# Optimization experiments

Hardware: AMD Instinct MI355X
Metric: run time of the kernel (lower is better)

The kernel has to match this reference:

```python
import jax, jax.numpy as jnp
import numpy as np

B, P, K = 32, 2048, 16
NHID, NCLS = 128, 10

def setup_inputs() -> dict:
    key = jax.random.key(0)
    ks = jax.random.split(key, 8)
    def w(k, shape):
        fan_in = shape[0]
        return jax.random.normal(k, shape, jnp.float32) / np.sqrt(fan_in)
    pos = jax.random.normal(ks[0], (B * P, 3), jnp.float32)
    batch = jnp.repeat(jnp.arange(B, dtype=jnp.int32), P)
    return dict(
        pos=pos, batch=batch,
        W1a=w(ks[1], (3 + 3, NHID)), b1a=jnp.zeros((NHID,), jnp.float32),
        W1b=w(ks[2], (NHID, NHID)), b1b=jnp.zeros((NHID,), jnp.float32),
        W2a=w(ks[3], (NHID + 3, NHID)), b2a=jnp.zeros((NHID,), jnp.float32),
        W2b=w(ks[4], (NHID, NHID)), b2b=jnp.zeros((NHID,), jnp.float32),
        Wc=w(ks[5], (NHID, NCLS)), bc=jnp.zeros((NCLS,), jnp.float32),
    )

def _gather(x, idx):
    # x: [B,P,C], idx: [B,P,K] -> [B,P,K,C]
    return jax.vmap(lambda xb, ib: xb[ib])(x, idx)

def _knn(posb):
    # posb: [B,P,3]; k nearest (incl. self, loop=True) per node -> [B,P,K]
    sq = jnp.sum(posb * posb, axis=-1)                      # [B,P]
    d2 = sq[:, :, None] + sq[:, None, :] - 2.0 * jnp.einsum('bpd,bqd->bpq', posb, posb)
    _, nbr = jax.lax.top_k(-d2, K)                          # [B,P,K]
    return nbr

def _pointnet_layer(h, posb, nbr, Wa, ba, Wb, bb):
    # message: concat(h_j, pos_j - pos_i) -> Linear -> ReLU -> Linear; aggr = max over K
    h_j = _gather(h, nbr)                                   # [B,P,K,C]
    rel = _gather(posb, nbr) - posb[:, :, None, :]          # [B,P,K,3]
    m = jnp.concatenate([h_j, rel], axis=-1)                # [B,P,K,C+3]
    m = jax.nn.relu(jnp.einsum('bpkc,cd->bpkd', m, Wa) + ba)
    m = jnp.einsum('bpkc,cd->bpkd', m, Wb) + bb
    return jnp.max(m, axis=2)                               # [B,P,NHID]

def reference(pos, batch, W1a, b1a, W1b, b1b, W2a, b2a, W2b, b2b, Wc, bc):
    posb = pos.reshape(B, P, 3)                             # batch is sorted, equal-size graphs
    nbr = _knn(posb)
    h = jax.nn.relu(_pointnet_layer(posb, posb, nbr, W1a, b1a, W1b, b1b))
    h = jax.nn.relu(_pointnet_layer(h, posb, nbr, W2a, b2a, W2b, b2b))
    g = jnp.max(h, axis=1)                                  # global_max_pool -> [B,NHID]
    return g @ Wc + bc                                      # [B,NCLS]
```

## Files before the change

### kernel.cpp

```cpp
#include <hip/hip_runtime.h>


typedef __bf16 bf16x8 __attribute__((ext_vector_type(8)));
typedef float  f32x4  __attribute__((ext_vector_type(4)));

#define LDSA __attribute__((aligned(16)))
#define WAVE_LDS_SYNC() __asm__ volatile("s_waitcnt lgkmcnt(0)" ::: "memory")

__global__ __launch_bounds__(512) void knn_kernel(const float* __restrict__ pos,
                                                  int* __restrict__ nbr) {
  __shared__ LDSA float4 P4[2048];
  const int blk = blockIdx.x;
  const int b = blk >> 5;
  const int tid = threadIdx.x;
  const size_t bbase = (size_t)b * 2048;
  for (int idx = tid; idx < 2048; idx += 512) {
    const float* pp = pos + (bbase + idx) * 3;
    float x = pp[0], y = pp[1], z = pp[2];
    P4[idx] = make_float4(-2.0f * x, -2.0f * y, -2.0f * z, fmaf(z, z, fmaf(y, y, x * x)));
  }
  __syncthreads();
  const int wave = tid >> 6, lane = tid & 63;
  const int p0 = (blk & 31) * 64 + wave * 8;
  const unsigned long long below = (1ull << lane) - 1ull;
  const float FINF = __uint_as_float(0x7F800000u);
  for (int it = 0; it < 8; ++it) {
    const int pl = p0 + it;
    const float4 Qp = P4[pl];
    const float Px = -0.5f * Qp.x, Py = -0.5f * Qp.y, Pz = -0.5f * Qp.z;
    float m1 = FINF, m2 = FINF, m3 = FINF;
    unsigned s1 = 0, s2 = 0, s3 = 0;
#pragma unroll 8
    for (int i = 0; i < 32; ++i) {
      int c = lane + (i << 6);
      float4 Q = P4[c];
      float d2 = fmaf(Px, Q.x, fmaf(Py, Q.y, fmaf(Pz, Q.z, Q.w)));
      bool c1 = d2 < m1, c2 = d2 < m2, c3 = d2 < m3;
      float n3 = __builtin_amdgcn_fmed3f(d2, m2, m3);
      float n2 = __builtin_amdgcn_fmed3f(d2, m1, m2);
      float n1 = fminf(d2, m1);
      s3 = c2 ? s2 : (c3 ? (unsigned)c : s3);
      s2 = c1 ? s1 : (c2 ? (unsigned)c : s2);
      s1 = c1 ? (unsigned)c : s1;
      m1 = n1; m2 = n2; m3 = n3;
    }
    unsigned u;
    unsigned k1, k2, k3;
    u = __float_as_uint(m1); k1 = ((int)u < 0) ? ~u : (u | 0x80000000u);
    u = __float_as_uint(m2); k2 = ((int)u < 0) ? ~u : (u | 0x80000000u);
    u = __float_as_uint(m3); k3 = ((int)u < 0) ? ~u : (u | 0x80000000u);
    unsigned v = 0;
#pragma unroll
    for (int bit = 31; bit >= 0; --bit) {
      unsigned t = v | (1u << bit);
      int cnt = __popcll(__ballot(k1 < t)) + __popcll(__ballot(k2 < t)) +
                __popcll(__ballot(k3 < t));
      if (cnt < 16) v = t;
    }
    const unsigned V = v;
    const long long outbase = ((long long)bbase + pl) * 16;
    if (__any(k3 < V)) {
      unsigned long long K1 = ((unsigned long long)k1 << 32) | s1;
      unsigned long long K2 = ((unsigned long long)k2 << 32) | s2;
      unsigned long long K3 = ((unsigned long long)k3 << 32) | s3;
      unsigned long long lastk = 0;
      for (int r = 0; r < 16; ++r) {
        unsigned long long k = K1, kmin = K1;
#pragma unroll
        for (int off = 1; off < 64; off <<= 1) {
          unsigned long long o = __shfl_xor(kmin, off);
          kmin = (o < kmin) ? o : kmin;
        }
        if (lane == r) nbr[outbase + r] = (int)(kmin & 0xFFFFFFFFull);
        if (k == kmin) { lastk = k; K1 = K2; K2 = K3; K3 = ~0ull; }
        if (r < 15 && __any(K1 == ~0ull)) {
          if (K1 == ~0ull) {
            unsigned long long best = ~0ull;
            for (int i = 0; i < 32; ++i) {
              int c = lane + (i << 6);
              float4 Q = P4[c];
              float d2 = fmaf(Px, Q.x, fmaf(Py, Q.y, fmaf(Pz, Q.z, Q.w)));
              unsigned uu = __float_as_uint(d2);
              uu = ((int)uu < 0) ? ~uu : (uu | 0x80000000u);
              unsigned long long kc = ((unsigned long long)uu << 32) | (unsigned)c;
              bool ok = (kc > lastk) & (kc < best);
              best = ok ? kc : best;
            }
            K1 = best;
          }
        }
      }
    } else {
      unsigned long long L1 = __ballot(k1 < V), L2 = __ballot(k2 < V), L3 = __ballot(k3 < V);
      unsigned long long E1 = __ballot(k1 == V), E2 = __ballot(k2 == V), E3 = __ballot(k3 == V);
      int cA = __popcll(L1), cB = cA + __popcll(L2), cT = cB + __popcll(L3);
      int eA = __popcll(E1), eB = eA + __popcll(E2);
      {
        bool lt = k1 < V, eq = k1 == V;
        int plt = __popcll(L1 & below);
        int peq = cT + __popcll(E1 & below);
        int p = lt ? plt : peq;
        if (lt || (eq && peq < 16)) nbr[outbase + p] = (int)s1;
      }
      {
        bool lt = k2 < V, eq = k2 == V;
        int plt = cA + __popcll(L2 & below);
        int peq = cT + eA + __popcll(E2 & below);
        int p = lt ? plt : peq;
        if (lt || (eq && peq < 16)) nbr[outbase + p] = (int)s2;
      }
      {
        bool lt = k3 < V, eq = k3 == V;
        int plt = cB + __popcll(L3 & below);
        int peq = cT + eB + __popcll(E3 & below);
        int p = lt ? plt : peq;
        if (lt || (eq && peq < 16)) nbr[outbase + p] = (int)s3;
      }
    }
  }
}

__global__ __launch_bounds__(256, 2) void layer1_kernel(
    const float* __restrict__ pos, const int* __restrict__ nbr,
    const float* __restrict__ W1a, const float* __restrict__ b1a,
    const float* __restrict__ W1b, const float* __restrict__ b1b,
    __bf16* __restrict__ h1e) {
  __shared__ LDSA char smem[34816];
  __bf16* Wbt = (__bf16*)smem;
  const int tid = threadIdx.x;
  for (int idx = tid; idx < 16384; idx += 256) {
    int k = idx >> 7, n = idx & 127;
    Wbt[n * 136 + k] = (__bf16)W1b[idx];
  }
  __syncthreads();
  const int wave = tid >> 6, lane = tid & 63;
  const int q = lane >> 4, c15 = lane & 15;
  bf16x8 bfr[8][4];
#pragma unroll
  for (int nt = 0; nt < 8; ++nt)
#pragma unroll
    for (int t = 0; t < 4; ++t)
      bfr[nt][t] = *(const bf16x8*)&Wbt[(nt * 16 + c15) * 136 + t * 32 + q * 8];
  __syncthreads();
  __bf16* mt = (__bf16*)smem + wave * 2176;
  float* base = (float*)(smem + 17408) + wave * 128;
  const int cb = lane & 7, k0 = lane >> 3, C0 = cb * 16;
  float4 s0h[4], s1h[4], s2h[4];
#pragma unroll
  for (int i = 0; i < 4; ++i) {
    float4 a0 = *(const float4*)&W1a[      C0 + 4 * i], r0 = *(const float4*)&W1a[384 + C0 + 4 * i];
    float4 a1 = *(const float4*)&W1a[128 + C0 + 4 * i], r1 = *(const float4*)&W1a[512 + C0 + 4 * i];
    float4 a2 = *(const float4*)&W1a[256 + C0 + 4 * i], r2 = *(const float4*)&W1a[640 + C0 + 4 * i];
    s0h[i] = make_float4(a0.x + r0.x, a0.y + r0.y, a0.z + r0.z, a0.w + r0.w);
    s1h[i] = make_float4(a1.x + r1.x, a1.y + r1.y, a1.z + r1.z, a1.w + r1.w);
    s2h[i] = make_float4(a2.x + r2.x, a2.y + r2.y, a2.z + r2.z, a2.w + r2.w);
  }
  const int c2 = lane * 2;
  const float br0a = W1a[384 + c2], br0b = W1a[384 + c2 + 1];
  const float br1a = W1a[512 + c2], br1b = W1a[512 + c2 + 1];
  const float br2a = W1a[640 + c2], br2b = W1a[640 + c2 + 1];
  const float ba0 = b1a[c2], ba1 = b1a[c2 + 1];
  const float bbi0 = b1b[q * 32 + c15], bbi1 = b1b[q * 32 + 16 + c15];
  const int blk = blockIdx.x, b = blk >> 5;
  const size_t bbase = (size_t)b * 2048;
  const int p0 = (blk & 31) * 64 + wave * 16;
  size_t node = bbase + p0;
  int j0 = nbr[node * 16 + k0];
  int j1 = nbr[node * 16 + k0 + 8];
  float px = pos[node * 3], py = pos[node * 3 + 1], pz = pos[node * 3 + 2];
  const float* t0 = pos + (bbase + j0) * 3;
  const float* t1 = pos + (bbase + j1) * 3;
  float xa = t0[0], ya = t0[1], za = t0[2];
  float xb = t1[0], yb = t1[1], zb = t1[2];
  for (int it = 0; it < 16; ++it) {
    const float xp = px, yp = py, zp = pz;
    const float xac = xa, yac = ya, zac = za;
    const float xbc = xb, ybc = yb, zbc = zb;
    const size_t nodec = node;
    if (it < 15) {
      node = nodec + 1;
      j0 = nbr[node * 16 + k0];
      j1 = nbr[node * 16 + k0 + 8];
      px = pos[node * 3]; py = pos[node * 3 + 1]; pz = pos[node * 3 + 2];
      const float* n0 = pos + (bbase + j0) * 3;
      const float* n1 = pos + (bbase + j1) * 3;
      xa = n0[0]; ya = n0[1]; za = n0[2];
      xb = n1[0]; yb = n1[1]; zb = n1[2];
    }
    float v0 = ba0 - fmaf(xp, br0a, fmaf(yp, br1a, zp * br2a));
    float v1 = ba1 - fmaf(xp, br0b, fmaf(yp, br1b, zp * br2b));
    *(float2*)&base[c2] = make_float2(v0, v1);
    WAVE_LDS_SYNC();
    float4 bb[4];
#pragma unroll
    for (int i = 0; i < 4; ++i) bb[i] = *(const float4*)&base[C0 + 4 * i];
#pragma unroll
    for (int r = 0; r < 2; ++r) {
      const float xj = r ? xbc : xac, yj = r ? ybc : yac, zj = r ? zbc : zac;
      bf16x8 o0, o1;
#pragma unroll
      for (int i = 0; i < 4; ++i) {
        float mx = fmaf(xj, s0h[i].x, fmaf(yj, s1h[i].x, fmaf(zj, s2h[i].x, bb[i].x)));
        float my = fmaf(xj, s0h[i].y, fmaf(yj, s1h[i].y, fmaf(zj, s2h[i].y, bb[i].y)));
        float mz = fmaf(xj, s0h[i].z, fmaf(yj, s1h[i].z, fmaf(zj, s2h[i].z, bb[i].z)));
        float mw = fmaf(xj, s0h[i].w, fmaf(yj, s1h[i].w, fmaf(zj, s2h[i].w, bb[i].w)));
        __bf16 e0 = (__bf16)fmaxf(mx, 0.f), e1 = (__bf16)fmaxf(my, 0.f);
        __bf16 e2 = (__bf16)fmaxf(mz, 0.f), e3 = (__bf16)fmaxf(mw, 0.f);
        if (i < 2) { o0[i * 4 + 0] = e0; o0[i * 4 + 1] = e1; o0[i * 4 + 2] = e2; o0[i * 4 + 3] = e3; }
        else { o1[(i - 2) * 4 + 0] = e0; o1[(i - 2) * 4 + 1] = e1; o1[(i - 2) * 4 + 2] = e2; o1[(i - 2) * 4 + 3] = e3; }
      }
      __bf16* dst = &mt[(k0 + 8 * r) * 136 + C0];
      *(bf16x8*)dst = o0;
      *(bf16x8*)(dst + 8) = o1;
    }
    WAVE_LDS_SYNC();
    bf16x8 af[4];
#pragma unroll
    for (int t = 0; t < 4; ++t)
      af[t] = *(const bf16x8*)&mt[c15 * 136 + t * 32 + q * 8];
    f32x4 acc[8] = {};
#pragma unroll
    for (int nt = 0; nt < 8; ++nt)
#pragma unroll
      for (int t = 0; t < 4; ++t)
        acc[nt] = __builtin_amdgcn_mfma_f32_16x16x32_bf16(af[t], bfr[nt][t], acc[nt], 0, 0, 0);
#pragma unroll
    for (int nt = 0; nt < 8; ++nt) {
      float m4 = fmaxf(fmaxf(acc[nt][0], acc[nt][1]), fmaxf(acc[nt][2], acc[nt][3]));
      m4 = fmaxf(m4, __shfl_xor(m4, 16));
      m4 = fmaxf(m4, __shfl_xor(m4, 32));
      if ((nt >> 1) == q) {
        float bias = (nt & 1) ? bbi1 : bbi0;
        h1e[nodec * 160 + nt * 16 + c15] = (__bf16)fmaxf(m4 + bias, 0.f);
      }
    }
    if (lane < 32) {
      __bf16 v = (__bf16)0.f;
      if (lane == 0) v = (__bf16)xp;
      else if (lane == 1) v = (__bf16)yp;
      else if (lane == 2) v = (__bf16)zp;
      h1e[nodec * 160 + 128 + lane] = v;
    }
  }
}

__global__ __launch_bounds__(256) void mid_gemm_kernel(
    const __bf16* __restrict__ h1e, const float* __restrict__ W2a,
    const float* __restrict__ b2a, __bf16* __restrict__ u2p) {
  __shared__ LDSA __bf16 Wt[128 * 168];
  const int tid = threadIdx.x;
  uint4 z = make_uint4(0, 0, 0, 0);
  for (int idx = tid; idx < 2688; idx += 256) ((uint4*)Wt)[idx] = z;
  __syncthreads();
  for (int idx = tid; idx < 131 * 32; idx += 256) {
    int k = idx >> 5, c4 = (idx & 31) * 4;
    float4 w = *(const float4*)&W2a[k * 128 + c4];
    Wt[(c4 + 0) * 168 + k] = (__bf16)w.x;
    Wt[(c4 + 1) * 168 + k] = (__bf16)w.y;
    Wt[(c4 + 2) * 168 + k] = (__bf16)w.z;
    Wt[(c4 + 3) * 168 + k] = (__bf16)w.w;
  }
  const int wave = tid >> 6, lane = tid & 63;
  const int q = lane >> 4, c15 = lane & 15;
  float biasr[8];
#pragma unroll
  for (int nt = 0; nt < 8; ++nt) biasr[nt] = b2a[nt * 16 + c15];
  __syncthreads();
  for (int tile = 0; tile < 4; ++tile) {
    const int row0 = blockIdx.x * 256 + tile * 64 + wave * 16;
    bf16x8 af[5];
#pragma unroll
    for (int t = 0; t < 5; ++t)
      af[t] = *(const bf16x8*)(h1e + (size_t)(row0 + c15) * 160 + t * 32 + q * 8);
    f32x4 acc[8] = {};
#pragma unroll
    for (int nt = 0; nt < 8; ++nt)
#pragma unroll
      for (int t = 0; t < 5; ++t) {
        bf16x8 bf = *(const bf16x8*)&Wt[(nt * 16 + c15) * 168 + t * 32 + q * 8];
        acc[nt] = __builtin_amdgcn_mfma_f32_16x16x32_bf16(af[t], bf, acc[nt], 0, 0, 0);
      }
#pragma unroll
    for (int nt = 0; nt < 8; ++nt) {
#pragma unroll
      for (int r = 0; r < 4; ++r)
        u2p[(size_t)(row0 + q * 4 + r) * 128 + nt * 16 + c15] = (__bf16)(acc[nt][r] + biasr[nt]);
    }
  }
}

__global__ __launch_bounds__(256, 2) void layer2_kernel(
    const float* __restrict__ pos, const int* __restrict__ nbr,
    const __bf16* __restrict__ u2p, const float* __restrict__ W2a,
    const float* __restrict__ W2b, const float* __restrict__ b2b,
    int* __restrict__ gG) {
  __shared__ LDSA char smem[34816];
  __shared__ int gpart[128];
  __bf16* Wbt = (__bf16*)smem;
  const int tid = threadIdx.x;
  for (int idx = tid; idx < 16384; idx += 256) {
    int k = idx >> 7, n = idx & 127;
    Wbt[n * 136 + k] = (__bf16)W2b[idx];
  }
  if (tid < 128) gpart[tid] = 0;
  __syncthreads();
  const int wave = tid >> 6, lane = tid & 63;
  const int q = lane >> 4, c15 = lane & 15;
  bf16x8 bfr[8][4];
#pragma unroll
  for (int nt = 0; nt < 8; ++nt)
#pragma unroll
    for (int t = 0; t < 4; ++t)
      bfr[nt][t] = *(const bf16x8*)&Wbt[(nt * 16 + c15) * 136 + t * 32 + q * 8];
  __syncthreads();
  __bf16* mt = (__bf16*)smem + wave * 2176;
  float* proj = (float*)(smem + 17408) + wave * 128;
  const int cb = lane & 7, k0 = lane >> 3, C0 = cb * 16;
  const int c2 = lane * 2;
  const float r0a = W2a[16384 + c2], r0b = W2a[16384 + c2 + 1];
  const float r1a = W2a[16512 + c2], r1b = W2a[16512 + c2 + 1];
  const float r2a = W2a[16640 + c2], r2b = W2a[16640 + c2 + 1];
  const float bbi0 = b2b[q * 32 + c15], bbi1 = b2b[q * 32 + 16 + c15];
  const int lb = blockIdx.x;
  const int xcd = lb & 7, slot = lb >> 3;
  const int b = xcd + 8 * (slot >> 5);
  const int bi = slot & 31;
  const size_t bbase = (size_t)b * 2048;
  const int p0 = bi * 64 + wave * 16;
  size_t node = bbase + p0;
  int j0 = nbr[node * 16 + k0];
  int j1 = nbr[node * 16 + k0 + 8];
  float px = pos[node * 3], py = pos[node * 3 + 1], pz = pos[node * 3 + 2];
  const __bf16* g0 = u2p + (size_t)(bbase + j0) * 128 + C0;
  const __bf16* g1 = u2p + (size_t)(bbase + j1) * 128 + C0;
  bf16x8 ua0 = *(const bf16x8*)g0, ua1 = *(const bf16x8*)(g0 + 8);
  bf16x8 ub0 = *(const bf16x8*)g1, ub1 = *(const bf16x8*)(g1 + 8);
  for (int it = 0; it < 16; ++it) {
    const float xp = px, yp = py, zp = pz;
    const bf16x8 ua0c = ua0, ua1c = ua1, ub0c = ub0, ub1c = ub1;
    const size_t nodec = node;
    if (it < 15) {
      node = nodec + 1;
      j0 = nbr[node * 16 + k0];
      j1 = nbr[node * 16 + k0 + 8];
      px = pos[node * 3]; py = pos[node * 3 + 1]; pz = pos[node * 3 + 2];
      const __bf16* n0 = u2p + (size_t)(bbase + j0) * 128 + C0;
      const __bf16* n1 = u2p + (size_t)(bbase + j1) * 128 + C0;
      ua0 = *(const bf16x8*)n0; ua1 = *(const bf16x8*)(n0 + 8);
      ub0 = *(const bf16x8*)n1; ub1 = *(const bf16x8*)(n1 + 8);
    }
    float v0 = fmaf(xp, r0a, fmaf(yp, r1a, zp * r2a));
    float v1 = fmaf(xp, r0b, fmaf(yp, r1b, zp * r2b));
    *(float2*)&proj[c2] = make_float2(v0, v1);
    WAVE_LDS_SYNC();
    float pj[16];
#pragma unroll
    for (int i = 0; i < 4; ++i) *(float4*)&pj[4 * i] = *(const float4*)&proj[C0 + 4 * i];
#pragma unroll
    for (int r = 0; r < 2; ++r) {
      bf16x8 u0 = r ? ub0c : ua0c, u1 = r ? ub1c : ua1c;
      bf16x8 o0, o1;
#pragma unroll
      for (int e = 0; e < 8; ++e) o0[e] = (__bf16)fmaxf((float)u0[e] - pj[e], 0.f);
#pragma unroll
      for (int e = 0; e < 8; ++e) o1[e] = (__bf16)fmaxf((float)u1[e] - pj[8 + e], 0.f);
      __bf16* dst = &mt[(k0 + 8 * r) * 136 + C0];
      *(bf16x8*)dst = o0;
      *(bf16x8*)(dst + 8) = o1;
    }
    WAVE_LDS_SYNC();
    bf16x8 af[4];
#pragma unroll
    for (int t = 0; t < 4; ++t)
      af[t] = *(const bf16x8*)&mt[c15 * 136 + t * 32 + q * 8];
    f32x4 acc[8] = {};
#pragma unroll
    for (int nt = 0; nt < 8; ++nt)
#pragma unroll
      for (int t = 0; t < 4; ++t)
        acc[nt] = __builtin_amdgcn_mfma_f32_16x16x32_bf16(af[t], bfr[nt][t], acc[nt], 0, 0, 0);
#pragma unroll
    for (int nt = 0; nt < 8; ++nt) {
      float m4 = fmaxf(fmaxf(acc[nt][0], acc[nt][1]), fmaxf(acc[nt][2], acc[nt][3]));
      m4 = fmaxf(m4, __shfl_xor(m4, 16));
      m4 = fmaxf(m4, __shfl_xor(m4, 32));
      if ((nt >> 1) == q) {
        float bias = (nt & 1) ? bbi1 : bbi0;
        float h = fmaxf(m4 + bias, 0.f);
        atomicMax(&gpart[nt * 16 + c15], __float_as_int(h));
      }
    }
  }
  __syncthreads();
  if (tid < 128) atomicMax(&gG[b * 128 + tid], gpart[tid]);
}

__global__ __launch_bounds__(64) void cls_kernel(const int* __restrict__ gG,
                                                 const float* __restrict__ Wc,
                                                 const float* __restrict__ bc,
                                                 float* __restrict__ out) {
  const int b = blockIdx.x, lane = threadIdx.x;
  float g1 = __int_as_float(gG[b * 128 + lane]);
  float g2 = __int_as_float(gG[b * 128 + 64 + lane]);
  float accn[10];
#pragma unroll
  for (int n = 0; n < 10; ++n)
    accn[n] = g1 * Wc[lane * 10 + n] + g2 * Wc[(64 + lane) * 10 + n];
#pragma unroll
  for (int n = 0; n < 10; ++n) {
#pragma unroll
    for (int off = 32; off >= 1; off >>= 1) accn[n] += __shfl_xor(accn[n], off);
  }
  if (lane == 0) {
#pragma unroll
    for (int n = 0; n < 10; ++n) out[b * 10 + n] = accn[n] + bc[n];
  }
}

extern "C" void kernel_launch(void* const* d_in, const int* in_sizes, int n_in,
                              void* d_out, int out_size, void* d_ws, size_t ws_size,
                              hipStream_t stream) {
  const float* pos = (const float*)d_in[0];
  const float* W1a = (const float*)d_in[2];
  const float* b1a = (const float*)d_in[3];
  const float* W1b = (const float*)d_in[4];
  const float* b1b = (const float*)d_in[5];
  const float* W2a = (const float*)d_in[6];
  const float* b2a = (const float*)d_in[7];
  const float* W2b = (const float*)d_in[8];
  const float* b2b = (const float*)d_in[9];
  const float* Wc  = (const float*)d_in[10];
  const float* bc  = (const float*)d_in[11];

  char* ws = (char*)d_ws;
  int*    nbr = (int*)ws;
  __bf16* h1e = (__bf16*)(ws + 4194304);
  __bf16* u2p = (__bf16*)(ws + 25165824);
  int*    gG  = (int*)(ws + 41943040);
  float*  out = (float*)d_out;

  hipMemsetAsync(gG, 0, 32 * 128 * sizeof(int), stream);
  knn_kernel<<<1024, 512, 0, stream>>>(pos, nbr);
  layer1_kernel<<<1024, 256, 0, stream>>>(pos, nbr, W1a, b1a, W1b, b1b, h1e);
  mid_gemm_kernel<<<256, 256, 0, stream>>>(h1e, W2a, b2a, u2p);
  layer2_kernel<<<1024, 256, 0, stream>>>(pos, nbr, u2p, W2a, W2b, b2b, gG);
  cls_kernel<<<32, 64, 0, stream>>>(gG, Wc, bc, out);
}
```

Baseline: 362.6 us.

## Split output channels across waves in layer kernels, block-wide per-node processing

Layer1 and layer2 now process one node at a time per block, with each wave computing 32 output channels instead of every wave handling its own nodes with all 128 channels. Because each wave keeps only a quarter of the W*b fragments, register use drops and the minimum-occupancy launch bound is removed. The message tile and the projection are double-buffered in LDS with a block-wide barrier per node. Layer2 keeps the running max in registers and does one global atomic at the end instead of per-node shared atomics. The mid GEMM now uses 512 threads with one tile per wave. The cost is a __syncthreads per node in place of wave-local waits.

```diff
diff --git a/kernel.cpp b/kernel.cpp
--- a/kernel.cpp
+++ b/kernel.cpp
@@ -5,7 +5,6 @@
 typedef float  f32x4  __attribute__((ext_vector_type(4)));
 
 #define LDSA __attribute__((aligned(16)))
-#define WAVE_LDS_SYNC() __asm__ volatile("s_waitcnt lgkmcnt(0)" ::: "memory")
 
 __global__ __launch_bounds__(512) void knn_kernel(const float* __restrict__ pos,
                                                   int* __restrict__ nbr) {
@@ -44,8 +43,7 @@
       s1 = c1 ? (unsigned)c : s1;
       m1 = n1; m2 = n2; m3 = n3;
     }
-    unsigned u;
-    unsigned k1, k2, k3;
+    unsigned u, k1, k2, k3;
     u = __float_as_uint(m1); k1 = ((int)u < 0) ? ~u : (u | 0x80000000u);
     u = __float_as_uint(m2); k2 = ((int)u < 0) ? ~u : (u | 0x80000000u);
     u = __float_as_uint(m3); k3 = ((int)u < 0) ? ~u : (u | 0x80000000u);
@@ -120,7 +118,7 @@
   }
 }
 
-__global__ __launch_bounds__(256, 2) void layer1_kernel(
+__global__ __launch_bounds__(256) void layer1_kernel(
     const float* __restrict__ pos, const int* __restrict__ nbr,
     const float* __restrict__ W1a, const float* __restrict__ b1a,
     const float* __restrict__ W1b, const float* __restrict__ b1b,
@@ -135,124 +133,112 @@
   __syncthreads();
   const int wave = tid >> 6, lane = tid & 63;
   const int q = lane >> 4, c15 = lane & 15;
-  bf16x8 bfr[8][4];
-#pragma unroll
-  for (int nt = 0; nt < 8; ++nt)
+  bf16x8 bfr[2][4];
+#pragma unroll
+  for (int i = 0; i < 2; ++i)
 #pragma unroll
     for (int t = 0; t < 4; ++t)
-      bfr[nt][t] = *(const bf16x8*)&Wbt[(nt * 16 + c15) * 136 + t * 32 + q * 8];
-  __syncthreads();
-  __bf16* mt = (__bf16*)smem + wave * 2176;
-  float* base = (float*)(smem + 17408) + wave * 128;
-  const int cb = lane & 7, k0 = lane >> 3, C0 = cb * 16;
-  float4 s0h[4], s1h[4], s2h[4];
-#pragma unroll
-  for (int i = 0; i < 4; ++i) {
-    float4 a0 = *(const float4*)&W1a[      C0 + 4 * i], r0 = *(const float4*)&W1a[384 + C0 + 4 * i];
-    float4 a1 = *(const float4*)&W1a[128 + C0 + 4 * i], r1 = *(const float4*)&W1a[512 + C0 + 4 * i];
-    float4 a2 = *(const float4*)&W1a[256 + C0 + 4 * i], r2 = *(const float4*)&W1a[640 + C0 + 4 * i];
-    s0h[i] = make_float4(a0.x + r0.x, a0.y + r0.y, a0.z + r0.z, a0.w + r0.w);
-    s1h[i] = make_float4(a1.x + r1.x, a1.y + r1.y, a1.z + r1.z, a1.w + r1.w);
-    s2h[i] = make_float4(a2.x + r2.x, a2.y + r2.y, a2.z + r2.z, a2.w + r2.w);
-  }
-  const int c2 = lane * 2;
-  const float br0a = W1a[384 + c2], br0b = W1a[384 + c2 + 1];
-  const float br1a = W1a[512 + c2], br1b = W1a[512 + c2 + 1];
-  const float br2a = W1a[640 + c2], br2b = W1a[640 + c2 + 1];
-  const float ba0 = b1a[c2], ba1 = b1a[c2 + 1];
-  const float bbi0 = b1b[q * 32 + c15], bbi1 = b1b[q * 32 + 16 + c15];
+      bfr[i][t] = *(const bf16x8*)&Wbt[((2 * wave + i) * 16 + c15) * 136 + t * 32 + q * 8];
+  __syncthreads();
+  __bf16* mt = (__bf16*)smem;
+  float* base = (float*)(smem + 8704);
+  const int nb = tid >> 4;
+  const int ch0 = (tid & 15) * 8;
+  float4 S0a, S0b, S1a, S1b, S2a, S2b;
+  {
+    float4 a, r;
+    a = *(const float4*)&W1a[ch0];           r = *(const float4*)&W1a[384 + ch0];
+    S0a = make_float4(a.x + r.x, a.y + r.y, a.z + r.z, a.w + r.w);
+    a = *(const float4*)&W1a[ch0 + 4];       r = *(const float4*)&W1a[388 + ch0];
+    S0b = make_float4(a.x + r.x, a.y + r.y, a.z + r.z, a.w + r.w);
+    a = *(const float4*)&W1a[128 + ch0];     r = *(const float4*)&W1a[512 + ch0];
+    S1a = make_float4(a.x + r.x, a.y + r.y, a.z + r.z, a.w + r.w);
+    a = *(const float4*)&W1a[132 + ch0];     r = *(const float4*)&W1a[516 + ch0];
+    S1b = make_float4(a.x + r.x, a.y + r.y, a.z + r.z, a.w + r.w);
+    a = *(const float4*)&W1a[256 + ch0];     r = *(const float4*)&W1a[640 + ch0];
+    S2a = make_float4(a.x + r.x, a.y + r.y, a.z + r.z, a.w + r.w);
+    a = *(const float4*)&W1a[260 + ch0];     r = *(const float4*)&W1a[644 + ch0];
+    S2b = make_float4(a.x + r.x, a.y + r.y, a.z + r.z, a.w + r.w);
+  }
+  const int cb = tid & 127;
+  const float br0 = W1a[384 + cb], br1 = W1a[512 + cb], br2 = W1a[640 + cb];
+  const float ba = b1a[cb];
+  const float bia0 = b1b[(2 * wave) * 16 + c15];
+  const float bia1 = b1b[(2 * wave + 1) * 16 + c15];
   const int blk = blockIdx.x, b = blk >> 5;
   const size_t bbase = (size_t)b * 2048;
-  const int p0 = (blk & 31) * 64 + wave * 16;
-  size_t node = bbase + p0;
-  int j0 = nbr[node * 16 + k0];
-  int j1 = nbr[node * 16 + k0 + 8];
-  float px = pos[node * 3], py = pos[node * 3 + 1], pz = pos[node * 3 + 2];
-  const float* t0 = pos + (bbase + j0) * 3;
-  const float* t1 = pos + (bbase + j1) * 3;
-  float xa = t0[0], ya = t0[1], za = t0[2];
-  float xb = t1[0], yb = t1[1], zb = t1[2];
-  for (int it = 0; it < 16; ++it) {
-    const float xp = px, yp = py, zp = pz;
-    const float xac = xa, yac = ya, zac = za;
-    const float xbc = xb, ybc = yb, zbc = zb;
-    const size_t nodec = node;
-    if (it < 15) {
-      node = nodec + 1;
-      j0 = nbr[node * 16 + k0];
-      j1 = nbr[node * 16 + k0 + 8];
-      px = pos[node * 3]; py = pos[node * 3 + 1]; pz = pos[node * 3 + 2];
-      const float* n0 = pos + (bbase + j0) * 3;
-      const float* n1 = pos + (bbase + j1) * 3;
-      xa = n0[0]; ya = n0[1]; za = n0[2];
-      xb = n1[0]; yb = n1[1]; zb = n1[2];
-    }
-    float v0 = ba0 - fmaf(xp, br0a, fmaf(yp, br1a, zp * br2a));
-    float v1 = ba1 - fmaf(xp, br0b, fmaf(yp, br1b, zp * br2b));
-    *(float2*)&base[c2] = make_float2(v0, v1);
-    WAVE_LDS_SYNC();
-    float4 bb[4];
-#pragma unroll
-    for (int i = 0; i < 4; ++i) bb[i] = *(const float4*)&base[C0 + 4 * i];
-#pragma unroll
-    for (int r = 0; r < 2; ++r) {
-      const float xj = r ? xbc : xac, yj = r ? ybc : yac, zj = r ? zbc : zac;
-      bf16x8 o0, o1;
-#pragma unroll
-      for (int i = 0; i < 4; ++i) {
-        float mx = fmaf(xj, s0h[i].x, fmaf(yj, s1h[i].x, fmaf(zj, s2h[i].x, bb[i].x)));
-        float my = fmaf(xj, s0h[i].y, fmaf(yj, s1h[i].y, fmaf(zj, s2h[i].y, bb[i].y)));
-        float mz = fmaf(xj, s0h[i].z, fmaf(yj, s1h[i].z, fmaf(zj, s2h[i].z, bb[i].z)));
-        float mw = fmaf(xj, s0h[i].w, fmaf(yj, s1h[i].w, fmaf(zj, s2h[i].w, bb[i].w)));
-        __bf16 e0 = (__bf16)fmaxf(mx, 0.f), e1 = (__bf16)fmaxf(my, 0.f);
-        __bf16 e2 = (__bf16)fmaxf(mz, 0.f), e3 = (__bf16)fmaxf(mw, 0.f);
-        if (i < 2) { o0[i * 4 + 0] = e0; o0[i * 4 + 1] = e1; o0[i * 4 + 2] = e2; o0[i * 4 + 3] = e3; }
-        else { o1[(i - 2) * 4 + 0] = e0; o1[(i - 2) * 4 + 1] = e1; o1[(i - 2) * 4 + 2] = e2; o1[(i - 2) * 4 + 3] = e3; }
-      }
-      __bf16* dst = &mt[(k0 + 8 * r) * 136 + C0];
-      *(bf16x8*)dst = o0;
-      *(bf16x8*)(dst + 8) = o1;
-    }
-    WAVE_LDS_SYNC();
+  size_t node = bbase + (blk & 31) * 64;
+  int jc = nbr[node * 16 + nb];
+  const float* pj0 = pos + (bbase + jc) * 3;
+  float xj = pj0[0], yj = pj0[1], zj = pj0[2];
+  float xp = pos[node * 3], yp = pos[node * 3 + 1], zp = pos[node * 3 + 2];
+  if (tid < 128) base[cb] = ba - fmaf(xp, br0, fmaf(yp, br1, zp * br2));
+  __syncthreads();
+  for (int it = 0; it < 64; ++it) {
+    const int cur = it & 1, nxt = cur ^ 1;
+    float xjn = 0.f, yjn = 0.f, zjn = 0.f, xpn = 0.f, ypn = 0.f, zpn = 0.f;
+    if (it < 63) {
+      const size_t node1 = node + 1;
+      const int jn = nbr[node1 * 16 + nb];
+      xpn = pos[node1 * 3]; ypn = pos[node1 * 3 + 1]; zpn = pos[node1 * 3 + 2];
+      const float* pjn = pos + (bbase + jn) * 3;
+      xjn = pjn[0]; yjn = pjn[1]; zjn = pjn[2];
+      if (tid < 128) base[nxt * 128 + cb] = ba - fmaf(xpn, br0, fmaf(ypn, br1, zpn * br2));
+    }
+    float4 bb0 = *(const float4*)&base[cur * 128 + ch0];
+    float4 bb1 = *(const float4*)&base[cur * 128 + ch0 + 4];
+    bf16x8 o;
+    o[0] = (__bf16)fmaxf(fmaf(xj, S0a.x, fmaf(yj, S1a.x, fmaf(zj, S2a.x, bb0.x))), 0.f);
+    o[1] = (__bf16)fmaxf(fmaf(xj, S0a.y, fmaf(yj, S1a.y, fmaf(zj, S2a.y, bb0.y))), 0.f);
+    o[2] = (__bf16)fmaxf(fmaf(xj, S0a.z, fmaf(yj, S1a.z, fmaf(zj, S2a.z, bb0.z))), 0.f);
+    o[3] = (__bf16)fmaxf(fmaf(xj, S0a.w, fmaf(yj, S1a.w, fmaf(zj, S2a.w, bb0.w))), 0.f);
+    o[4] = (__bf16)fmaxf(fmaf(xj, S0b.x, fmaf(yj, S1b.x, fmaf(zj, S2b.x, bb1.x))), 0.f);
+    o[5] = (__bf16)fmaxf(fmaf(xj, S0b.y, fmaf(yj, S1b.y, fmaf(zj, S2b.y, bb1.y))), 0.f);
+    o[6] = (__bf16)fmaxf(fmaf(xj, S0b.z, fmaf(yj, S1b.z, fmaf(zj, S2b.z, bb1.z))), 0.f);
+    o[7] = (__bf16)fmaxf(fmaf(xj, S0b.w, fmaf(yj, S1b.w, fmaf(zj, S2b.w, bb1.w))), 0.f);
+    *(bf16x8*)&mt[cur * 2176 + nb * 136 + ch0] = o;
+    __syncthreads();
     bf16x8 af[4];
 #pragma unroll
     for (int t = 0; t < 4; ++t)
-      af[t] = *(const bf16x8*)&mt[c15 * 136 + t * 32 + q * 8];
-    f32x4 acc[8] = {};
-#pragma unroll
-    for (int nt = 0; nt < 8; ++nt)
+      af[t] = *(const bf16x8*)&mt[cur * 2176 + c15 * 136 + t * 32 + q * 8];
+    f32x4 acc[2] = {};
+#pragma unroll
+    for (int i = 0; i < 2; ++i)
 #pragma unroll
       for (int t = 0; t < 4; ++t)
-        acc[nt] = __builtin_amdgcn_mfma_f32_16x16x32_bf16(af[t], bfr[nt][t], acc[nt], 0, 0, 0);
-#pragma unroll
-    for (int nt = 0; nt < 8; ++nt) {
-      float m4 = fmaxf(fmaxf(acc[nt][0], acc[nt][1]), fmaxf(acc[nt][2], acc[nt][3]));
+        acc[i] = __builtin_amdgcn_mfma_f32_16x16x32_bf16(af[t], bfr[i][t], acc[i], 0, 0, 0);
+#pragma unroll
+    for (int i = 0; i < 2; ++i) {
+      float m4 = fmaxf(fmaxf(acc[i][0], acc[i][1]), fmaxf(acc[i][2], acc[i][3]));
       m4 = fmaxf(m4, __shfl_xor(m4, 16));
       m4 = fmaxf(m4, __shfl_xor(m4, 32));
-      if ((nt >> 1) == q) {
-        float bias = (nt & 1) ? bbi1 : bbi0;
-        h1e[nodec * 160 + nt * 16 + c15] = (__bf16)fmaxf(m4 + bias, 0.f);
+      if (q == i) {
+        float bias = i ? bia1 : bia0;
+        h1e[node * 160 + (2 * wave + i) * 16 + c15] = (__bf16)fmaxf(m4 + bias, 0.f);
       }
     }
-    if (lane < 32) {
+    if (tid < 32) {
       __bf16 v = (__bf16)0.f;
-      if (lane == 0) v = (__bf16)xp;
-      else if (lane == 1) v = (__bf16)yp;
-      else if (lane == 2) v = (__bf16)zp;
-      h1e[nodec * 160 + 128 + lane] = v;
-    }
-  }
-}
-
-__global__ __launch_bounds__(256) void mid_gemm_kernel(
+      if (tid == 0) v = (__bf16)xp;
+      else if (tid == 1) v = (__bf16)yp;
+      else if (tid == 2) v = (__bf16)zp;
+      h1e[node * 160 + 128 + tid] = v;
+    }
+    node += 1;
+    xj = xjn; yj = yjn; zj = zjn; xp = xpn; yp = ypn; zp = zpn;
+  }
+}
+
+__global__ __launch_bounds__(512) void mid_gemm_kernel(
     const __bf16* __restrict__ h1e, const float* __restrict__ W2a,
     const float* __restrict__ b2a, __bf16* __restrict__ u2p) {
   __shared__ LDSA __bf16 Wt[128 * 168];
   const int tid = threadIdx.x;
   uint4 z = make_uint4(0, 0, 0, 0);
-  for (int idx = tid; idx < 2688; idx += 256) ((uint4*)Wt)[idx] = z;
-  __syncthreads();
-  for (int idx = tid; idx < 131 * 32; idx += 256) {
+  for (int idx = tid; idx < 2688; idx += 512) ((uint4*)Wt)[idx] = z;
+  __syncthreads();
+  for (int idx = tid; idx < 131 * 32; idx += 512) {
     int k = idx >> 5, c4 = (idx & 31) * 4;
     float4 w = *(const float4*)&W2a[k * 128 + c4];
     Wt[(c4 + 0) * 168 + k] = (__bf16)w.x;
@@ -266,133 +252,119 @@
 #pragma unroll
   for (int nt = 0; nt < 8; ++nt) biasr[nt] = b2a[nt * 16 + c15];
   __syncthreads();
-  for (int tile = 0; tile < 4; ++tile) {
-    const int row0 = blockIdx.x * 256 + tile * 64 + wave * 16;
-    bf16x8 af[5];
-#pragma unroll
-    for (int t = 0; t < 5; ++t)
-      af[t] = *(const bf16x8*)(h1e + (size_t)(row0 + c15) * 160 + t * 32 + q * 8);
-    f32x4 acc[8] = {};
-#pragma unroll
-    for (int nt = 0; nt < 8; ++nt)
-#pragma unroll
-      for (int t = 0; t < 5; ++t) {
-        bf16x8 bf = *(const bf16x8*)&Wt[(nt * 16 + c15) * 168 + t * 32 + q * 8];
-        acc[nt] = __builtin_amdgcn_mfma_f32_16x16x32_bf16(af[t], bf, acc[nt], 0, 0, 0);
-      }
-#pragma unroll
-    for (int nt = 0; nt < 8; ++nt) {
-#pragma unroll
-      for (int r = 0; r < 4; ++r)
-        u2p[(size_t)(row0 + q * 4 + r) * 128 + nt * 16 + c15] = (__bf16)(acc[nt][r] + biasr[nt]);
-    }
-  }
-}
-
-__global__ __launch_bounds__(256, 2) void layer2_kernel(
+  const int row0 = blockIdx.x * 128 + wave * 16;
+  bf16x8 af[5];
+#pragma unroll
+  for (int t = 0; t < 5; ++t)
+    af[t] = *(const bf16x8*)(h1e + (size_t)(row0 + c15) * 160 + t * 32 + q * 8);
+  f32x4 acc[8] = {};
+#pragma unroll
+  for (int nt = 0; nt < 8; ++nt)
+#pragma unroll
+    for (int t = 0; t < 5; ++t) {
+      bf16x8 bf = *(const bf16x8*)&Wt[(nt * 16 + c15) * 168 + t * 32 + q * 8];
+      acc[nt] = __builtin_amdgcn_mfma_f32_16x16x32_bf16(af[t], bf, acc[nt], 0, 0, 0);
+    }
+#pragma unroll
+  for (int nt = 0; nt < 8; ++nt) {
+#pragma unroll
+    for (int r = 0; r < 4; ++r)
+      u2p[(size_t)(row0 + q * 4 + r) * 128 + nt * 16 + c15] = (__bf16)(acc[nt][r] + biasr[nt]);
+  }
+}
+
+__global__ __launch_bounds__(256) void layer2_kernel(
     const float* __restrict__ pos, const int* __restrict__ nbr,
     const __bf16* __restrict__ u2p, const float* __restrict__ W2a,
     const float* __restrict__ W2b, const float* __restrict__ b2b,
     int* __restrict__ gG) {
   __shared__ LDSA char smem[34816];
-  __shared__ int gpart[128];
   __bf16* Wbt = (__bf16*)smem;
   const int tid = threadIdx.x;
   for (int idx = tid; idx < 16384; idx += 256) {
     int k = idx >> 7, n = idx & 127;
     Wbt[n * 136 + k] = (__bf16)W2b[idx];
   }
-  if (tid < 128) gpart[tid] = 0;
   __syncthreads();
   const int wave = tid >> 6, lane = tid & 63;
   const int q = lane >> 4, c15 = lane & 15;
-  bf16x8 bfr[8][4];
-#pragma unroll
-  for (int nt = 0; nt < 8; ++nt)
+  bf16x8 bfr[2][4];
+#pragma unroll
+  for (int i = 0; i < 2; ++i)
 #pragma unroll
     for (int t = 0; t < 4; ++t)
-      bfr[nt][t] = *(const bf16x8*)&Wbt[(nt * 16 + c15) * 136 + t * 32 + q * 8];
-  __syncthreads();
-  __bf16* mt = (__bf16*)smem + wave * 2176;
-  float* proj = (float*)(smem + 17408) + wave * 128;
-  const int cb = lane & 7, k0 = lane >> 3, C0 = cb * 16;
-  const int c2 = lane * 2;
-  const float r0a = W2a[16384 + c2], r0b = W2a[16384 + c2 + 1];
-  const float r1a = W2a[16512 + c2], r1b = W2a[16512 + c2 + 1];
-  const float r2a = W2a[16640 + c2], r2b = W2a[16640 + c2 + 1];
-  const float bbi0 = b2b[q * 32 + c15], bbi1 = b2b[q * 32 + 16 + c15];
+      bfr[i][t] = *(const bf16x8*)&Wbt[((2 * wave + i) * 16 + c15) * 136 + t * 32 + q * 8];
+  __syncthreads();
+  __bf16* mt = (__bf16*)smem;
+  float* proj = (float*)(smem + 8704);
+  const int nb = tid >> 4;
+  const int ch0 = (tid & 15) * 8;
+  const int cb = tid & 127;
+  const float r0 = W2a[16384 + cb], r1 = W2a[16512 + cb], r2 = W2a[16640 + cb];
+  const float bia0 = b2b[(2 * wave) * 16 + c15];
+  const float bia1 = b2b[(2 * wave + 1) * 16 + c15];
   const int lb = blockIdx.x;
   const int xcd = lb & 7, slot = lb >> 3;
   const int b = xcd + 8 * (slot >> 5);
   const int bi = slot & 31;
   const size_t bbase = (size_t)b * 2048;
-  const int p0 = bi * 64 + wave * 16;
-  size_t node = bbase + p0;
-  int j0 = nbr[node * 16 + k0];
-  int j1 = nbr[node * 16 + k0 + 8];
-  float px = pos[node * 3], py = pos[node * 3 + 1], pz = pos[node * 3 + 2];
-  const __bf16* g0 = u2p + (size_t)(bbase + j0) * 128 + C0;
-  const __bf16* g1 = u2p + (size_t)(bbase + j1) * 128 + C0;
-  bf16x8 ua0 = *(const bf16x8*)g0, ua1 = *(const bf16x8*)(g0 + 8);
-  bf16x8 ub0 = *(const bf16x8*)g1, ub1 = *(const bf16x8*)(g1 + 8);
-  for (int it = 0; it < 16; ++it) {
-    const float xp = px, yp = py, zp = pz;
-    const bf16x8 ua0c = ua0, ua1c = ua1, ub0c = ub0, ub1c = ub1;
-    const size_t nodec = node;
-    if (it < 15) {
-      node = nodec + 1;
-      j0 = nbr[node * 16 + k0];
-      j1 = nbr[node * 16 + k0 + 8];
-      px = pos[node * 3]; py = pos[node * 3 + 1]; pz = pos[node * 3 + 2];
-      const __bf16* n0 = u2p + (size_t)(bbase + j0) * 128 + C0;
-      const __bf16* n1 = u2p + (size_t)(bbase + j1) * 128 + C0;
-      ua0 = *(const bf16x8*)n0; ua1 = *(const bf16x8*)(n0 + 8);
-      ub0 = *(const bf16x8*)n1; ub1 = *(const bf16x8*)(n1 + 8);
-    }
-    float v0 = fmaf(xp, r0a, fmaf(yp, r1a, zp * r2a));
-    float v1 = fmaf(xp, r0b, fmaf(yp, r1b, zp * r2b));
-    *(float2*)&proj[c2] = make_float2(v0, v1);
-    WAVE_LDS_SYNC();
-    float pj[16];
-#pragma unroll
-    for (int i = 0; i < 4; ++i) *(float4*)&pj[4 * i] = *(const float4*)&proj[C0 + 4 * i];
-#pragma unroll
-    for (int r = 0; r < 2; ++r) {
-      bf16x8 u0 = r ? ub0c : ua0c, u1 = r ? ub1c : ua1c;
-      bf16x8 o0, o1;
-#pragma unroll
-      for (int e = 0; e < 8; ++e) o0[e] = (__bf16)fmaxf((float)u0[e] - pj[e], 0.f);
-#pragma unroll
-      for (int e = 0; e < 8; ++e) o1[e] = (__bf16)fmaxf((float)u1[e] - pj[8 + e], 0.f);
-      __bf16* dst = &mt[(k0 + 8 * r) * 136 + C0];
-      *(bf16x8*)dst = o0;
-      *(bf16x8*)(dst + 8) = o1;
-    }
-    WAVE_LDS_SYNC();
+  size_t node = bbase + bi * 64;
+  int jc = nbr[node * 16 + nb];
+  bf16x8 uc = *(const bf16x8*)(u2p + (size_t)(bbase + jc) * 128 + ch0);
+  float xp = pos[node * 3], yp = pos[node * 3 + 1], zp = pos[node * 3 + 2];
+  if (tid < 128) proj[cb] = fmaf(xp, r0, fmaf(yp, r1, zp * r2));
+  __syncthreads();
+  float rmax0 = 0.f, rmax1 = 0.f;
+  for (int it = 0; it < 64; ++it) {
+    const int cur = it & 1, nxt = cur ^ 1;
+    bf16x8 un = {};
+    if (it < 63) {
+      const size_t node1 = node + 1;
+      const int jn = nbr[node1 * 16 + nb];
+      un = *(const bf16x8*)(u2p + (size_t)(bbase + jn) * 128 + ch0);
+      const float xpn = pos[node1 * 3], ypn = pos[node1 * 3 + 1], zpn = pos[node1 * 3 + 2];
+      if (tid < 128) proj[nxt * 128 + cb] = fmaf(xpn, r0, fmaf(ypn, r1, zpn * r2));
+    }
+    float4 p0 = *(const float4*)&proj[cur * 128 + ch0];
+    float4 p1 = *(const float4*)&proj[cur * 128 + ch0 + 4];
+    bf16x8 o;
+    o[0] = (__bf16)fmaxf((float)uc[0] - p0.x, 0.f);
+    o[1] = (__bf16)fmaxf((float)uc[1] - p0.y, 0.f);
+    o[2] = (__bf16)fmaxf((float)uc[2] - p0.z, 0.f);
+    o[3] = (__bf16)fmaxf((float)uc[3] - p0.w, 0.f);
+    o[4] = (__bf16)fmaxf((float)uc[4] - p1.x, 0.f);
+    o[5] = (__bf16)fmaxf((float)uc[5] - p1.y, 0.f);
+    o[6] = (__bf16)fmaxf((float)uc[6] - p1.z, 0.f);
+    o[7] = (__bf16)fmaxf((float)uc[7] - p1.w, 0.f);
+    *(bf16x8*)&mt[cur * 2176 + nb * 136 + ch0] = o;
+    __syncthreads();
     bf16x8 af[4];
 #pragma unroll
     for (int t = 0; t < 4; ++t)
-      af[t] = *(const bf16x8*)&mt[c15 * 136 + t * 32 + q * 8];
-    f32x4 acc[8] = {};
-#pragma unroll
-    for (int nt = 0; nt < 8; ++nt)
+      af[t] = *(const bf16x8*)&mt[cur * 2176 + c15 * 136 + t * 32 + q * 8];
+    f32x4 acc[2] = {};
+#pragma unroll
+    for (int i = 0; i < 2; ++i)
 #pragma unroll
       for (int t = 0; t < 4; ++t)
-        acc[nt] = __builtin_amdgcn_mfma_f32_16x16x32_bf16(af[t], bfr[nt][t], acc[nt], 0, 0, 0);
-#pragma unroll
-    for (int nt = 0; nt < 8; ++nt) {
-      float m4 = fmaxf(fmaxf(acc[nt][0], acc[nt][1]), fmaxf(acc[nt][2], acc[nt][3]));
+        acc[i] = __builtin_amdgcn_mfma_f32_16x16x32_bf16(af[t], bfr[i][t], acc[i], 0, 0, 0);
+    {
+      float m4 = fmaxf(fmaxf(acc[0][0], acc[0][1]), fmaxf(acc[0][2], acc[0][3]));
       m4 = fmaxf(m4, __shfl_xor(m4, 16));
       m4 = fmaxf(m4, __shfl_xor(m4, 32));
-      if ((nt >> 1) == q) {
-        float bias = (nt & 1) ? bbi1 : bbi0;
-        float h = fmaxf(m4 + bias, 0.f);
-        atomicMax(&gpart[nt * 16 + c15], __float_as_int(h));
-      }
-    }
-  }
-  __syncthreads();
-  if (tid < 128) atomicMax(&gG[b * 128 + tid], gpart[tid]);
+      rmax0 = fmaxf(rmax0, fmaxf(m4 + bia0, 0.f));
+    }
+    {
+      float m4 = fmaxf(fmaxf(acc[1][0], acc[1][1]), fmaxf(acc[1][2], acc[1][3]));
+      m4 = fmaxf(m4, __shfl_xor(m4, 16));
+      m4 = fmaxf(m4, __shfl_xor(m4, 32));
+      rmax1 = fmaxf(rmax1, fmaxf(m4 + bia1, 0.f));
+    }
+    node += 1;
+    uc = un;
+  }
+  if (q == 0) atomicMax(&gG[b * 128 + (2 * wave) * 16 + c15], __float_as_int(rmax0));
+  if (q == 1) atomicMax(&gG[b * 128 + (2 * wave + 1) * 16 + c15], __float_as_int(rmax1));
 }
 
 __global__ __launch_bounds__(64) void cls_kernel(const int* __restrict__ gG,
@@ -442,7 +414,7 @@
   hipMemsetAsync(gG, 0, 32 * 128 * sizeof(int), stream);
   knn_kernel<<<1024, 512, 0, stream>>>(pos, nbr);
   layer1_kernel<<<1024, 256, 0, stream>>>(pos, nbr, W1a, b1a, W1b, b1b, h1e);
-  mid_gemm_kernel<<<256, 256, 0, stream>>>(h1e, W2a, b2a, u2p);
+  mid_gemm_kernel<<<512, 512, 0, stream>>>(h1e, W2a, b2a, u2p);
   layer2_kernel<<<1024, 256, 0, stream>>>(pos, nbr, u2p, W2a, W2b, b2b, gG);
   cls_kernel<<<32, 64, 0, stream>>>(gG, Wc, bc, out);
 }
```

Result: faster. 352.9 us (-2.7%).
